# Optimization experiments

Measured on AMD Instinct MI355X. Metric: run time of the kernel, lower is better.

Reference implementation:

```python
import jax, jax.numpy as jnp
import numpy as np

B, S, L, D, H, F, V = 8, 1024, 12, 768, 12, 3072, 21128
TITLE_LEN, CONTENTS_LEN = 64, 960
DH = D // H
NEG_INF = -1e9


def setup_inputs() -> dict:
    key = jax.random.key(0)
    ks = jax.random.split(key, 14)
    p = lambda k, shape: (0.02 * jax.random.normal(k, shape)).astype(jnp.float32)
    return {
        "x": jax.random.randint(ks[0], (B, S), 0, V),
        "y": jax.random.randint(ks[1], (B, CONTENTS_LEN), 0, V),
        "word_emb": p(ks[2], (V, D)),
        "pos_emb": p(ks[3], (S, D)),
        "type_emb": p(ks[4], (2, D)),
        "emb_ln_g": jnp.ones((D,), jnp.float32),
        "emb_ln_b": jnp.zeros((D,), jnp.float32),
        "Wq": p(ks[5], (L, D, D)), "bq": jnp.zeros((L, D), jnp.float32),
        "Wk": p(ks[6], (L, D, D)), "bk": jnp.zeros((L, D), jnp.float32),
        "Wv": p(ks[7], (L, D, D)), "bv": jnp.zeros((L, D), jnp.float32),
        "Wo": p(ks[8], (L, D, D)), "bo": jnp.zeros((L, D), jnp.float32),
        "ln1_g": jnp.ones((L, D), jnp.float32), "ln1_b": jnp.zeros((L, D), jnp.float32),
        "W1": p(ks[9], (L, D, F)), "b1": jnp.zeros((L, F), jnp.float32),
        "W2": p(ks[10], (L, F, D)), "b2": jnp.zeros((L, D), jnp.float32),
        "ln2_g": jnp.ones((L, D), jnp.float32), "ln2_b": jnp.zeros((L, D), jnp.float32),
        "cls_W": p(ks[11], (D, V)), "cls_b": jnp.zeros((V,), jnp.float32),
    }


def _ln(x, g, b):
    m = x.mean(-1, keepdims=True)
    v = jnp.mean((x - m) ** 2, -1, keepdims=True)
    return (x - m) * jax.lax.rsqrt(v + 1e-12) * g + b


def _forward(x, y, word_emb, pos_emb, type_emb, emb_ln_g, emb_ln_b,
             Wq, bq, Wk, bk, Wv, bv, Wo, bo, ln1_g, ln1_b,
             W1, b1, W2, b2, ln2_g, ln2_b, cls_W, cls_b):
    # prefix-LM mask: causal (tril) except fully-visible title block [S,S]
    mask = jnp.tril(jnp.ones((S, S), jnp.float32))
    mask = mask.at[:TITLE_LEN, :TITLE_LEN].set(1.0)
    bias = (1.0 - mask) * NEG_INF  # additive attention bias

    h = word_emb[x] + pos_emb[None, :, :] + type_emb[0]  # [B,S,D]
    h = _ln(h, emb_ln_g, emb_ln_b)

    scale = 1.0 / np.sqrt(DH).astype(np.float32)

    def step(h, p):
        Wq_, bq_, Wk_, bk_, Wv_, bv_, Wo_, bo_, g1, bb1, W1_, bf1, W2_, bf2, g2, bb2 = p
        q = (h @ Wq_ + bq_).reshape(B, S, H, DH)
        k = (h @ Wk_ + bk_).reshape(B, S, H, DH)
        v = (h @ Wv_ + bv_).reshape(B, S, H, DH)
        scores = jnp.einsum('bqhd,bkhd->bhqk', q, k) * scale + bias  # [B,H,S,S]
        a = jax.nn.softmax(scores, axis=-1)
        ctx = jnp.einsum('bhqk,bkhd->bqhd', a, v).reshape(B, S, D)
        h = _ln(h + ctx @ Wo_ + bo_, g1, bb1)
        ffn = jax.nn.gelu(h @ W1_ + bf1, approximate=False) @ W2_ + bf2
        h = _ln(h + ffn, g2, bb2)
        return h, None

    h, _ = jax.lax.scan(step, h, (Wq, bq, Wk, bk, Wv, bv, Wo, bo,
                                  ln1_g, ln1_b, W1, b1, W2, b2, ln2_g, ln2_b))

    logits = h[:, -CONTENTS_LEN:, :] @ cls_W + cls_b  # [B,C,V]
    logp = jax.nn.log_softmax(logits, axis=-1)
    valid = (y != -100)
    yc = jnp.where(valid, y, 0)
    nll = -jnp.take_along_axis(logp, yc[..., None], axis=-1)[..., 0]
    return jnp.sum(nll * valid) / jnp.maximum(jnp.sum(valid), 1)


def reference(x, y, word_emb, pos_emb, type_emb, emb_ln_g, emb_ln_b,
              Wq, bq, Wk, bk, Wv, bv, Wo, bo, ln1_g, ln1_b,
              W1, b1, W2, b2, ln2_g, ln2_b, cls_W, cls_b):
    return _forward(x, y, word_emb, pos_emb, type_emb, emb_ln_g, emb_ln_b,
                    Wq, bq, Wk, bk, Wv, bv, Wo, bo, ln1_g, ln1_b,
                    W1, b1, W2, b2, ln2_g, ln2_b, cls_W, cls_b)
```

## Files before the change

kernel.cpp:

```cpp
#include <hip/hip_runtime.h>

#define BB 8
#define SS 1024
#define LL 12
#define DD 768
#define HH 12
#define FF 3072
#define VV 21128
#define DH 64
#define CLEN 960
#define NROWS (BB * CLEN)
#define TOKS (BB * SS)
#define NQKV 2304
#define QKW 1536

typedef __attribute__((ext_vector_type(8))) short bh8;
typedef __attribute__((ext_vector_type(4))) float f32x4;
typedef __attribute__((ext_vector_type(4))) unsigned short us4;

__device__ __forceinline__ float bf2f(unsigned short u) {
    union { unsigned int i; float f; } c; c.i = ((unsigned int)u) << 16; return c.f;
}
__device__ __forceinline__ unsigned short f2bf(float f) {
    union { float f; unsigned int i; } c; c.f = f;
    unsigned int r = c.i + 0x7fffu + ((c.i >> 16) & 1u);
    return (unsigned short)(r >> 16);
}

#define GLOAD16(gsrc, ldst)                                                              \
    __builtin_amdgcn_global_load_lds((const __attribute__((address_space(1))) unsigned int*)(gsrc), \
                                     (__attribute__((address_space(3))) unsigned int*)(ldst), 16, 0, 0)

__device__ __forceinline__ float bsum256(float v, float* red) {
#pragma unroll
    for (int o = 32; o; o >>= 1) v += __shfl_down(v, o);
    if ((threadIdx.x & 63) == 0) red[threadIdx.x >> 6] = v;
    __syncthreads();
    float r = red[0] + red[1] + red[2] + red[3];
    __syncthreads();
    return r;
}

__global__ void transpose_f32_bf16(const float* __restrict__ in, unsigned short* __restrict__ out,
                                   int R, int C) {
    __shared__ float tile[32][33];
    int c0 = blockIdx.x << 5, r0 = blockIdx.y << 5;
    int tx = threadIdx.x, ty = threadIdx.y;
    for (int i = ty; i < 32; i += 8) {
        int r = r0 + i, c = c0 + tx;
        if (r < R && c < C) tile[i][tx] = in[(size_t)r * C + c];
    }
    __syncthreads();
    for (int i = ty; i < 32; i += 8) {
        int oc = c0 + i, orr = r0 + tx;
        if (oc < C && orr < R) out[(size_t)oc * R + orr] = f2bf(tile[tx][i]);
    }
}

__global__ void transpose_layer(const float* __restrict__ Wq, const float* __restrict__ Wk,
                                const float* __restrict__ Wv, const float* __restrict__ Wo,
                                const float* __restrict__ W1, const float* __restrict__ W2,
                                unsigned short* __restrict__ wqkvT, unsigned short* __restrict__ woT,
                                unsigned short* __restrict__ w1T, unsigned short* __restrict__ w2T) {
    __shared__ float tile[32][33];
    int t = blockIdx.x;
    const float* src;
    unsigned short* dst;
    int R, C, txt, tt;
    if (t < 1728) {
        int which = t / 576; tt = t % 576;
        src = which == 0 ? Wq : (which == 1 ? Wk : Wv);
        dst = wqkvT + (size_t)which * DD * DD; R = DD; C = DD; txt = 24;
    } else if (t < 2304) {
        tt = t - 1728; src = Wo; dst = woT; R = DD; C = DD; txt = 24;
    } else if (t < 4608) {
        tt = t - 2304; src = W1; dst = w1T; R = DD; C = FF; txt = 96;
    } else {
        tt = t - 4608; src = W2; dst = w2T; R = FF; C = DD; txt = 24;
    }
    int c0 = (tt % txt) << 5, r0 = (tt / txt) << 5;
    int tx = threadIdx.x, ty = threadIdx.y;
    for (int i = ty; i < 32; i += 8) tile[i][tx] = src[(size_t)(r0 + i) * C + c0 + tx];
    __syncthreads();
    for (int i = ty; i < 32; i += 8) dst[(size_t)(c0 + i) * R + r0 + tx] = f2bf(tile[tx][i]);
}

__global__ void concat_bias_all(const float* __restrict__ bq, const float* __restrict__ bk,
                                const float* __restrict__ bv, float* __restrict__ out) {
    int i = blockIdx.x * 256 + threadIdx.x;
    if (i >= LL * NQKV) return;
    int l = i / NQKV, c = i % NQKV;
    float v = c < DD ? bq[(size_t)l * DD + c]
                     : (c < 2 * DD ? bk[(size_t)l * DD + c - DD] : bv[(size_t)l * DD + c - 2 * DD]);
    out[i] = v;
}

__global__ __launch_bounds__(256) void embed_ln(const int* __restrict__ x, const float* __restrict__ we,
                                                const float* __restrict__ pe, const float* __restrict__ te,
                                                const float* __restrict__ g, const float* __restrict__ be,
                                                unsigned short* __restrict__ hb) {
    int row = blockIdx.x;
    int s = row & (SS - 1);
    int tok = x[row];
    int tid = threadIdx.x;
    __shared__ float red[4];
    float v[3];
#pragma unroll
    for (int i = 0; i < 3; i++) {
        int c = tid + i * 256;
        v[i] = we[(size_t)tok * DD + c] + pe[(size_t)s * DD + c] + te[c];
    }
    float mean = bsum256(v[0] + v[1] + v[2], red) * (1.f / DD);
    float d0 = v[0] - mean, d1 = v[1] - mean, d2 = v[2] - mean;
    float var = bsum256(d0 * d0 + d1 * d1 + d2 * d2, red) * (1.f / DD);
    float inv = rsqrtf(var + 1e-12f);
    size_t base = (size_t)row * DD;
#pragma unroll
    for (int i = 0; i < 3; i++) {
        int c = tid + i * 256;
        hb[base + c] = f2bf((v[i] - mean) * inv * g[c] + be[c]);
    }
}

__global__ __launch_bounds__(256) void add_ln(const unsigned short* __restrict__ res,
                                              const unsigned short* __restrict__ t,
                                              const float* __restrict__ g, const float* __restrict__ be,
                                              unsigned short* __restrict__ outb) {
    int row = blockIdx.x;
    int tid = threadIdx.x;
    __shared__ float red[4];
    size_t base = (size_t)row * DD;
    float v[3];
#pragma unroll
    for (int i = 0; i < 3; i++) {
        int c = tid + i * 256;
        v[i] = bf2f(res[base + c]) + bf2f(t[base + c]);
    }
    float mean = bsum256(v[0] + v[1] + v[2], red) * (1.f / DD);
    float d0 = v[0] - mean, d1 = v[1] - mean, d2 = v[2] - mean;
    float var = bsum256(d0 * d0 + d1 * d1 + d2 * d2, red) * (1.f / DD);
    float inv = rsqrtf(var + 1e-12f);
#pragma unroll
    for (int i = 0; i < 3; i++) {
        int c = tid + i * 256;
        outb[base + c] = f2bf((v[i] - mean) * inv * g[c] + be[c]);
    }
}

template <int MODE>
__global__ __launch_bounds__(256) void gemm128(const unsigned short* __restrict__ A,
                                               const unsigned short* __restrict__ BT,
                                               const float* __restrict__ bias, void* __restrict__ Cp,
                                               int M, int N, int K, int ldc,
                                               unsigned short* __restrict__ vt_out,
                                               const int* __restrict__ yv,
                                               float* __restrict__ stS, float* __restrict__ stT) {
    __shared__ __align__(16) unsigned short As[2][128 * 32];
    __shared__ __align__(16) unsigned short Bs[2][128 * 32];
    const int tid = threadIdx.x;
    const int lane = tid & 63, w = tid >> 6;
    const int fr = lane & 15, fg = lane >> 4;
    const int wr = w >> 1, wc = w & 1;
    const int m0 = blockIdx.y << 7, n0 = blockIdx.x << 7;
    const int srow = lane >> 2;
    const int skcol = (lane & 3) << 3;

    int arow0 = m0 + (w * 2 + 0) * 16 + srow;
    int arow1 = m0 + (w * 2 + 1) * 16 + srow;
    int brow0 = n0 + (w * 2 + 0) * 16 + srow;
    int brow1 = n0 + (w * 2 + 1) * 16 + srow;
    if (brow0 >= N) brow0 = N - 1;
    if (brow1 >= N) brow1 = N - 1;
    const unsigned short* aptr0 = A + (size_t)arow0 * K + skcol;
    const unsigned short* aptr1 = A + (size_t)arow1 * K + skcol;
    const unsigned short* bptr0 = BT + (size_t)brow0 * K + skcol;
    const unsigned short* bptr1 = BT + (size_t)brow1 * K + skcol;

    auto stage = [&](int bf, int k0) {
        GLOAD16(aptr0 + k0, &As[bf][(w * 2 + 0) * 512]);
        GLOAD16(aptr1 + k0, &As[bf][(w * 2 + 1) * 512]);
        GLOAD16(bptr0 + k0, &Bs[bf][(w * 2 + 0) * 512]);
        GLOAD16(bptr1 + k0, &Bs[bf][(w * 2 + 1) * 512]);
    };

    f32x4 acc[4][4] = {};
    stage(0, 0);
    __syncthreads();
    int cur = 0;
    for (int k0 = 0; k0 < K; k0 += 32) {
        if (k0 + 32 < K) stage(cur ^ 1, k0 + 32);
        bh8 a[4], b[4];
#pragma unroll
        for (int mi = 0; mi < 4; mi++) a[mi] = *(const bh8*)&As[cur][(wr * 64 + mi * 16 + fr) * 32 + fg * 8];
#pragma unroll
        for (int ni = 0; ni < 4; ni++) b[ni] = *(const bh8*)&Bs[cur][(wc * 64 + ni * 16 + fr) * 32 + fg * 8];
        __builtin_amdgcn_s_setprio(1);
#pragma unroll
        for (int mi = 0; mi < 4; mi++)
#pragma unroll
            for (int ni = 0; ni < 4; ni++)
                acc[mi][ni] = __builtin_amdgcn_mfma_f32_16x16x32_bf16(a[mi], b[ni], acc[mi][ni], 0, 0, 0);
        __builtin_amdgcn_s_setprio(0);
        __syncthreads();
        cur ^= 1;
    }

    unsigned short* Cb = (unsigned short*)Cp;
#pragma unroll
    for (int mi = 0; mi < 4; mi++) {
        int rbase = m0 + wr * 64 + mi * 16 + fg * 4;
        if (MODE == 3) {
            float e[4] = {0.f, 0.f, 0.f, 0.f};
            int yr[4];
#pragma unroll
            for (int r = 0; r < 4; r++) yr[r] = yv[rbase + r];
#pragma unroll
            for (int ni = 0; ni < 4; ni++) {
                int col = n0 + wc * 64 + ni * 16 + fr;
                if (col < N) {
                    float bb = bias[col];
#pragma unroll
                    for (int r = 0; r < 4; r++) {
                        float v = acc[mi][ni][r] + bb;
                        e[r] += __expf(v);
                        if (col == yr[r]) stT[rbase + r] = v;
                    }
                }
            }
#pragma unroll
            for (int r = 0; r < 4; r++) {
#pragma unroll
                for (int off = 1; off < 16; off <<= 1) e[r] += __shfl_xor(e[r], off);
                if (fr == 0) atomicAdd(&stS[rbase + r], e[r]);
            }
        } else {
#pragma unroll
            for (int ni = 0; ni < 4; ni++) {
                int col = n0 + wc * 64 + ni * 16 + fr;
                if (MODE == 4) {
                    float bb = bias[col];
                    if (col < 2 * DD) {
#pragma unroll
                        for (int r = 0; r < 4; r++)
                            Cb[(size_t)(rbase + r) * QKW + col] = f2bf(acc[mi][ni][r] + bb);
                    } else {
                        int g = col - 2 * DD, h = g >> 6, d = g & 63;
                        int bi = rbase >> 10, s0 = rbase & 1023;
                        us4 val;
#pragma unroll
                        for (int r = 0; r < 4; r++) val[r] = f2bf(acc[mi][ni][r] + bb);
                        *(us4*)&vt_out[(((size_t)bi * HH + h) * DH + d) * SS + s0] = val;
                    }
                } else if (col < N) {
                    float bb = bias[col];
#pragma unroll
                    for (int r = 0; r < 4; r++) {
                        float v = acc[mi][ni][r] + bb;
                        if (MODE == 2) v = 0.5f * v * (1.0f + erff(v * 0.70710678118f));
                        Cb[(size_t)(rbase + r) * ldc + col] = f2bf(v);
                    }
                }
            }
        }
    }
}

__global__ __launch_bounds__(256) void flash_attn(const unsigned short* __restrict__ qkbuf,
                                                  const unsigned short* __restrict__ VT,
                                                  unsigned short* __restrict__ ctxb) {
    const int qt = (int)gridDim.x - 1 - blockIdx.x;
    const int h = blockIdx.y, b = blockIdx.z;
    const int tid = threadIdx.x;
    const int lane = tid & 63, w = tid >> 6;
    const int fr = lane & 15, fg = lane >> 4;
    __shared__ unsigned short Qs[64][68];
    __shared__ unsigned short Ks[64][68];
    __shared__ unsigned short Vt[64][68];
    __shared__ unsigned short Ps[4][16][68];

    const int srow = tid >> 2, sd0 = (tid & 3) << 4;
    {
        const unsigned short* src = qkbuf + (size_t)(b * SS + qt * 64 + srow) * QKW + h * 64 + sd0;
        *(bh8*)&Qs[srow][sd0] = *(const bh8*)src;
        *(bh8*)&Qs[srow][sd0 + 8] = *(const bh8*)(src + 8);
    }

    const unsigned short* kbase = qkbuf + (size_t)(b * SS + srow) * QKW + DD + h * 64 + sd0;
    const unsigned short* vbase = VT + (((size_t)b * HH + h) * DH + srow) * SS + sd0;

    bh8 kr0, kr1, vr0, vr1;
    auto ld_reg = [&](int kt) {
        const unsigned short* ks = kbase + (size_t)(kt * 64) * QKW;
        kr0 = *(const bh8*)ks;
        kr1 = *(const bh8*)(ks + 8);
        const unsigned short* vs = vbase + kt * 64;
        vr0 = *(const bh8*)vs;
        vr1 = *(const bh8*)(vs + 8);
    };

    f32x4 o[4] = {};
    float m[4], l[4];
#pragma unroll
    for (int r = 0; r < 4; r++) { m[r] = -3e30f; l[r] = 0.f; }

    const int nkt = (qt == 0) ? 1 : qt + 1;
    ld_reg(0);
    for (int kt = 0; kt < nkt; kt++) {
        __syncthreads();
        *(bh8*)&Ks[srow][sd0] = kr0;
        *(bh8*)&Ks[srow][sd0 + 8] = kr1;
        *(bh8*)&Vt[srow][sd0] = vr0;
        *(bh8*)&Vt[srow][sd0 + 8] = vr1;
        if (kt + 1 < nkt) ld_reg(kt + 1);
        __syncthreads();

        f32x4 s[4] = {};
        bh8 a0 = *(const bh8*)&Qs[w * 16 + fr][fg * 8];
        bh8 a1 = *(const bh8*)&Qs[w * 16 + fr][32 + fg * 8];
        __builtin_amdgcn_s_setprio(1);
#pragma unroll
        for (int cf = 0; cf < 4; cf++) {
            bh8 b0 = *(const bh8*)&Ks[cf * 16 + fr][fg * 8];
            bh8 b1 = *(const bh8*)&Ks[cf * 16 + fr][32 + fg * 8];
            s[cf] = __builtin_amdgcn_mfma_f32_16x16x32_bf16(a0, b0, s[cf], 0, 0, 0);
            s[cf] = __builtin_amdgcn_mfma_f32_16x16x32_bf16(a1, b1, s[cf], 0, 0, 0);
        }
        __builtin_amdgcn_s_setprio(0);

        const bool diag = (qt > 0) && (kt == qt);
#pragma unroll
        for (int cf = 0; cf < 4; cf++) {
#pragma unroll
            for (int r = 0; r < 4; r++) {
                float v = s[cf][r] * 0.125f;
                if (diag) {
                    int key = cf * 16 + fr;
                    int qrow = w * 16 + fg * 4 + r;
                    if (key > qrow) v = -1e30f;
                }
                s[cf][r] = v;
            }
        }
        float sc[4], mn[4];
#pragma unroll
        for (int r = 0; r < 4; r++) {
            float v = fmaxf(fmaxf(s[0][r], s[1][r]), fmaxf(s[2][r], s[3][r]));
#pragma unroll
            for (int off = 1; off < 16; off <<= 1) v = fmaxf(v, __shfl_xor(v, off));
            mn[r] = fmaxf(m[r], v);
            sc[r] = __expf(m[r] - mn[r]);
            m[r] = mn[r];
        }
#pragma unroll
        for (int cf = 0; cf < 4; cf++) {
#pragma unroll
            for (int r = 0; r < 4; r++) s[cf][r] = __expf(s[cf][r] - mn[r]);
        }
#pragma unroll
        for (int r = 0; r < 4; r++) {
            float v = s[0][r] + s[1][r] + s[2][r] + s[3][r];
#pragma unroll
            for (int off = 1; off < 16; off <<= 1) v += __shfl_xor(v, off);
            l[r] = l[r] * sc[r] + v;
        }
#pragma unroll
        for (int df = 0; df < 4; df++) {
#pragma unroll
            for (int r = 0; r < 4; r++) o[df][r] *= sc[r];
        }
#pragma unroll
        for (int cf = 0; cf < 4; cf++) {
#pragma unroll
            for (int r = 0; r < 4; r++) Ps[w][fg * 4 + r][cf * 16 + fr] = f2bf(s[cf][r]);
        }
        bh8 pa0 = *(const bh8*)&Ps[w][fr][fg * 8];
        bh8 pa1 = *(const bh8*)&Ps[w][fr][32 + fg * 8];
        __builtin_amdgcn_s_setprio(1);
#pragma unroll
        for (int df = 0; df < 4; df++) {
            bh8 vb0 = *(const bh8*)&Vt[df * 16 + fr][fg * 8];
            bh8 vb1 = *(const bh8*)&Vt[df * 16 + fr][32 + fg * 8];
            o[df] = __builtin_amdgcn_mfma_f32_16x16x32_bf16(pa0, vb0, o[df], 0, 0, 0);
            o[df] = __builtin_amdgcn_mfma_f32_16x16x32_bf16(pa1, vb1, o[df], 0, 0, 0);
        }
        __builtin_amdgcn_s_setprio(0);
    }
#pragma unroll
    for (int df = 0; df < 4; df++) {
#pragma unroll
        for (int r = 0; r < 4; r++) {
            int q = qt * 64 + w * 16 + fg * 4 + r;
            float v = o[df][r] / l[r];
            ctxb[(((size_t)b * SS + q) * HH + h) * DH + df * 16 + fr] = f2bf(v);
        }
    }
}

__global__ void gather_rows(const unsigned short* __restrict__ hb, unsigned short* __restrict__ hc) {
    int idx = blockIdx.x * 256 + threadIdx.x;
    if (idx >= NROWS * (DD / 8)) return;
    int g = idx / (DD / 8), c8 = (idx % (DD / 8)) * 8;
    int b = g / CLEN, cc = g % CLEN;
    *(bh8*)&hc[(size_t)g * DD + c8] = *(const bh8*)&hb[((size_t)(b * SS + 64 + cc)) * DD + c8];
}

__global__ void init_state(float* stS, float* stT) {
    int i = blockIdx.x * 256 + threadIdx.x;
    if (i < NROWS) { stS[i] = 0.f; stT[i] = 0.f; }
}

__global__ __launch_bounds__(256) void final_reduce(const float* __restrict__ stS,
                                                    const float* __restrict__ stT, const int* __restrict__ y,
                                                    float* __restrict__ out) {
    int tid = threadIdx.x;
    float s = 0.f, c = 0.f;
    for (int i = tid; i < NROWS; i += 256) {
        if (y[i] != -100) {
            s += logf(stS[i]) - stT[i];
            c += 1.f;
        }
    }
    __shared__ float red[4];
    float gs = bsum256(s, red);
    float gc = bsum256(c, red);
    if (tid == 0) out[0] = gs / fmaxf(gc, 1.f);
}

extern "C" void kernel_launch(void* const* d_in, const int* in_sizes, int n_in,
                              void* d_out, int out_size, void* d_ws, size_t ws_size,
                              hipStream_t stream) {
    const int* x = (const int*)d_in[0];
    const int* y = (const int*)d_in[1];
    const float* we = (const float*)d_in[2];
    const float* pe = (const float*)d_in[3];
    const float* te = (const float*)d_in[4];
    const float* eg = (const float*)d_in[5];
    const float* eb = (const float*)d_in[6];
    const float* Wq = (const float*)d_in[7];
    const float* bq = (const float*)d_in[8];
    const float* Wk = (const float*)d_in[9];
    const float* bk = (const float*)d_in[10];
    const float* Wv = (const float*)d_in[11];
    const float* bv = (const float*)d_in[12];
    const float* Wo = (const float*)d_in[13];
    const float* bo = (const float*)d_in[14];
    const float* g1 = (const float*)d_in[15];
    const float* b1n = (const float*)d_in[16];
    const float* W1 = (const float*)d_in[17];
    const float* b1 = (const float*)d_in[18];
    const float* W2 = (const float*)d_in[19];
    const float* b2 = (const float*)d_in[20];
    const float* g2 = (const float*)d_in[21];
    const float* b2n = (const float*)d_in[22];
    const float* clsW = (const float*)d_in[23];
    const float* clsb = (const float*)d_in[24];
    float* out = (float*)d_out;

    char* ws = (char*)d_ws;
    size_t off = 0;
    auto alloc = [&](size_t n) {
        void* p = ws + off;
        off += n;
        off = (off + 255) & ~(size_t)255;
        return p;
    };
    unsigned short* hb   = (unsigned short*)alloc((size_t)TOKS * DD * 2);
    unsigned short* h1b  = (unsigned short*)alloc((size_t)TOKS * DD * 2);
    unsigned short* tmpb = (unsigned short*)alloc((size_t)TOKS * DD * 2);
    unsigned short* qkbuf = (unsigned short*)alloc((size_t)TOKS * QKW * 2);
    unsigned short* vtb  = (unsigned short*)alloc((size_t)TOKS * DD * 2);
    unsigned short* ctxb = (unsigned short*)alloc((size_t)TOKS * DD * 2);
    unsigned short* ffnb = (unsigned short*)alloc((size_t)TOKS * FF * 2);
    unsigned short* wqkvT = (unsigned short*)alloc((size_t)NQKV * DD * 2);
    unsigned short* woT = (unsigned short*)alloc((size_t)DD * DD * 2);
    unsigned short* w1T = (unsigned short*)alloc((size_t)DD * FF * 2);
    unsigned short* w2T = (unsigned short*)alloc((size_t)DD * FF * 2);
    unsigned short* clsT = (unsigned short*)alloc((size_t)VV * DD * 2);
    unsigned short* hc = (unsigned short*)alloc((size_t)NROWS * DD * 2);
    float* bqkv = (float*)alloc((size_t)LL * NQKV * 4);
    float* stS = (float*)alloc(NROWS * 4);
    float* stT = (float*)alloc(NROWS * 4);

    dim3 tb(32, 8);
    transpose_f32_bf16<<<dim3((VV + 31) / 32, DD / 32), tb, 0, stream>>>(clsW, clsT, DD, VV);
    concat_bias_all<<<(LL * NQKV + 255) / 256, 256, 0, stream>>>(bq, bk, bv, bqkv);
    embed_ln<<<TOKS, 256, 0, stream>>>(x, we, pe, te, eg, eb, hb);

    for (int l = 0; l < LL; l++) {
        transpose_layer<<<6912, tb, 0, stream>>>(Wq + (size_t)l * DD * DD, Wk + (size_t)l * DD * DD,
                                                 Wv + (size_t)l * DD * DD, Wo + (size_t)l * DD * DD,
                                                 W1 + (size_t)l * DD * FF, W2 + (size_t)l * FF * DD,
                                                 wqkvT, woT, w1T, w2T);

        gemm128<4><<<dim3(NQKV / 128, TOKS / 128), 256, 0, stream>>>(hb, wqkvT, bqkv + (size_t)l * NQKV,
                                                                     qkbuf, TOKS, NQKV, DD, NQKV, vtb,
                                                                     nullptr, nullptr, nullptr);

        flash_attn<<<dim3(SS / 64, HH, BB), 256, 0, stream>>>(qkbuf, vtb, ctxb);

        gemm128<1><<<dim3(DD / 128, TOKS / 128), 256, 0, stream>>>(ctxb, woT, bo + (size_t)l * DD, tmpb,
                                                                   TOKS, DD, DD, DD, nullptr,
                                                                   nullptr, nullptr, nullptr);
        add_ln<<<TOKS, 256, 0, stream>>>(hb, tmpb, g1 + (size_t)l * DD, b1n + (size_t)l * DD, h1b);

        gemm128<2><<<dim3(FF / 128, TOKS / 128), 256, 0, stream>>>(h1b, w1T, b1 + (size_t)l * FF, ffnb,
                                                                   TOKS, FF, DD, FF, nullptr,
                                                                   nullptr, nullptr, nullptr);
        gemm128<1><<<dim3(DD / 128, TOKS / 128), 256, 0, stream>>>(ffnb, w2T, b2 + (size_t)l * DD, tmpb,
                                                                   TOKS, DD, FF, DD, nullptr,
                                                                   nullptr, nullptr, nullptr);
        add_ln<<<TOKS, 256, 0, stream>>>(h1b, tmpb, g2 + (size_t)l * DD, b2n + (size_t)l * DD, hb);
    }

    gather_rows<<<(NROWS * (DD / 8) + 255) / 256, 256, 0, stream>>>(hb, hc);
    init_state<<<(NROWS + 255) / 256, 256, 0, stream>>>(stS, stT);
    gemm128<3><<<dim3((VV + 127) / 128, NROWS / 128), 256, 0, stream>>>(hc, clsT, clsb, nullptr,
                                                                        NROWS, VV, DD, VV, nullptr,
                                                                        y, stS, stT);
    final_reduce<<<1, 256, 0, stream>>>(stS, stT, y, out);
}
```

Baseline: 4.653 ms.

## Swizzle GEMM tile order for XCD/L2 locality and pair causal attention q-tiles

GEMM blocks are remapped so that consecutive blocks on each XCD cover a band of M tiles across N, with the goal of better L2 reuse of A and B tiles. Flash attention now launches half as many blocks, and each processes a short and a long q-tile (15-bx and bx) to balance the causal triangular work across blocks. The trade-offs are extra index arithmetic, and half the attention grid size, which may reduce occupancy and parallelism.

```diff
diff --git a/kernel.cpp b/kernel.cpp
--- a/kernel.cpp
+++ b/kernel.cpp
@@ -151,7 +151,7 @@
 __global__ __launch_bounds__(256) void gemm128(const unsigned short* __restrict__ A,
                                                const unsigned short* __restrict__ BT,
                                                const float* __restrict__ bias, void* __restrict__ Cp,
-                                               int M, int N, int K, int ldc,
+                                               int M, int N, int K, int ldc, int SM,
                                                unsigned short* __restrict__ vt_out,
                                                const int* __restrict__ yv,
                                                float* __restrict__ stS, float* __restrict__ stT) {
@@ -161,7 +161,17 @@
     const int lane = tid & 63, w = tid >> 6;
     const int fr = lane & 15, fg = lane >> 4;
     const int wr = w >> 1, wc = w & 1;
-    const int m0 = blockIdx.y << 7, n0 = blockIdx.x << 7;
+
+    const int Nt = gridDim.x;
+    const int flat = blockIdx.y * Nt + blockIdx.x;
+    const int per8 = (Nt * gridDim.y) >> 3;
+    const int virt = (flat & 7) * per8 + (flat >> 3);
+    const int bandSz = SM * Nt;
+    const int band = virt / bandSz, rem = virt - band * bandSz;
+    const int nt = rem / SM;
+    const int mt = band * SM + (rem - nt * SM);
+    const int m0 = mt << 7, n0 = nt << 7;
+
     const int srow = lane >> 2;
     const int skcol = (lane & 3) << 3;
 
@@ -268,7 +278,7 @@
 __global__ __launch_bounds__(256) void flash_attn(const unsigned short* __restrict__ qkbuf,
                                                   const unsigned short* __restrict__ VT,
                                                   unsigned short* __restrict__ ctxb) {
-    const int qt = (int)gridDim.x - 1 - blockIdx.x;
+    const int bx = blockIdx.x;
     const int h = blockIdx.y, b = blockIdx.z;
     const int tid = threadIdx.x;
     const int lane = tid & 63, w = tid >> 6;
@@ -279,12 +289,6 @@
     __shared__ unsigned short Ps[4][16][68];
 
     const int srow = tid >> 2, sd0 = (tid & 3) << 4;
-    {
-        const unsigned short* src = qkbuf + (size_t)(b * SS + qt * 64 + srow) * QKW + h * 64 + sd0;
-        *(bh8*)&Qs[srow][sd0] = *(const bh8*)src;
-        *(bh8*)&Qs[srow][sd0 + 8] = *(const bh8*)(src + 8);
-    }
-
     const unsigned short* kbase = qkbuf + (size_t)(b * SS + srow) * QKW + DD + h * 64 + sd0;
     const unsigned short* vbase = VT + (((size_t)b * HH + h) * DH + srow) * SS + sd0;
 
@@ -298,100 +302,110 @@
         vr1 = *(const bh8*)(vs + 8);
     };
 
-    f32x4 o[4] = {};
-    float m[4], l[4];
-#pragma unroll
-    for (int r = 0; r < 4; r++) { m[r] = -3e30f; l[r] = 0.f; }
-
-    const int nkt = (qt == 0) ? 1 : qt + 1;
-    ld_reg(0);
-    for (int kt = 0; kt < nkt; kt++) {
+    for (int half = 0; half < 2; half++) {
+        const int qt = (half == 0) ? 15 - bx : bx;
         __syncthreads();
-        *(bh8*)&Ks[srow][sd0] = kr0;
-        *(bh8*)&Ks[srow][sd0 + 8] = kr1;
-        *(bh8*)&Vt[srow][sd0] = vr0;
-        *(bh8*)&Vt[srow][sd0 + 8] = vr1;
-        if (kt + 1 < nkt) ld_reg(kt + 1);
-        __syncthreads();
-
-        f32x4 s[4] = {};
-        bh8 a0 = *(const bh8*)&Qs[w * 16 + fr][fg * 8];
-        bh8 a1 = *(const bh8*)&Qs[w * 16 + fr][32 + fg * 8];
-        __builtin_amdgcn_s_setprio(1);
-#pragma unroll
-        for (int cf = 0; cf < 4; cf++) {
-            bh8 b0 = *(const bh8*)&Ks[cf * 16 + fr][fg * 8];
-            bh8 b1 = *(const bh8*)&Ks[cf * 16 + fr][32 + fg * 8];
-            s[cf] = __builtin_amdgcn_mfma_f32_16x16x32_bf16(a0, b0, s[cf], 0, 0, 0);
-            s[cf] = __builtin_amdgcn_mfma_f32_16x16x32_bf16(a1, b1, s[cf], 0, 0, 0);
+        {
+            const unsigned short* src = qkbuf + (size_t)(b * SS + qt * 64 + srow) * QKW + h * 64 + sd0;
+            *(bh8*)&Qs[srow][sd0] = *(const bh8*)src;
+            *(bh8*)&Qs[srow][sd0 + 8] = *(const bh8*)(src + 8);
         }
-        __builtin_amdgcn_s_setprio(0);
-
-        const bool diag = (qt > 0) && (kt == qt);
-#pragma unroll
-        for (int cf = 0; cf < 4; cf++) {
+
+        f32x4 o[4] = {};
+        float m[4], l[4];
+#pragma unroll
+        for (int r = 0; r < 4; r++) { m[r] = -3e30f; l[r] = 0.f; }
+
+        const int nkt = (qt == 0) ? 1 : qt + 1;
+        ld_reg(0);
+        for (int kt = 0; kt < nkt; kt++) {
+            __syncthreads();
+            *(bh8*)&Ks[srow][sd0] = kr0;
+            *(bh8*)&Ks[srow][sd0 + 8] = kr1;
+            *(bh8*)&Vt[srow][sd0] = vr0;
+            *(bh8*)&Vt[srow][sd0 + 8] = vr1;
+            if (kt + 1 < nkt) ld_reg(kt + 1);
+            __syncthreads();
+
+            f32x4 s[4] = {};
+            bh8 a0 = *(const bh8*)&Qs[w * 16 + fr][fg * 8];
+            bh8 a1 = *(const bh8*)&Qs[w * 16 + fr][32 + fg * 8];
+            __builtin_amdgcn_s_setprio(1);
+#pragma unroll
+            for (int cf = 0; cf < 4; cf++) {
+                bh8 b0 = *(const bh8*)&Ks[cf * 16 + fr][fg * 8];
+                bh8 b1 = *(const bh8*)&Ks[cf * 16 + fr][32 + fg * 8];
+                s[cf] = __builtin_amdgcn_mfma_f32_16x16x32_bf16(a0, b0, s[cf], 0, 0, 0);
+                s[cf] = __builtin_amdgcn_mfma_f32_16x16x32_bf16(a1, b1, s[cf], 0, 0, 0);
+            }
+            __builtin_amdgcn_s_setprio(0);
+
+            const bool diag = (qt > 0) && (kt == qt);
+#pragma unroll
+            for (int cf = 0; cf < 4; cf++) {
+#pragma unroll
+                for (int r = 0; r < 4; r++) {
+                    float v = s[cf][r] * 0.125f;
+                    if (diag) {
+                        int key = cf * 16 + fr;
+                        int qrow = w * 16 + fg * 4 + r;
+                        if (key > qrow) v = -1e30f;
+                    }
+                    s[cf][r] = v;
+                }
+            }
+            float sc[4], mn[4];
 #pragma unroll
             for (int r = 0; r < 4; r++) {
-                float v = s[cf][r] * 0.125f;
-                if (diag) {
-                    int key = cf * 16 + fr;
-                    int qrow = w * 16 + fg * 4 + r;
-                    if (key > qrow) v = -1e30f;
-                }
-                s[cf][r] = v;
-            }
+                float v = fmaxf(fmaxf(s[0][r], s[1][r]), fmaxf(s[2][r], s[3][r]));
+#pragma unroll
+                for (int off = 1; off < 16; off <<= 1) v = fmaxf(v, __shfl_xor(v, off));
+                mn[r] = fmaxf(m[r], v);
+                sc[r] = __expf(m[r] - mn[r]);
+                m[r] = mn[r];
+            }
+#pragma unroll
+            for (int cf = 0; cf < 4; cf++) {
+#pragma unroll
+                for (int r = 0; r < 4; r++) s[cf][r] = __expf(s[cf][r] - mn[r]);
+            }
+#pragma unroll
+            for (int r = 0; r < 4; r++) {
+                float v = s[0][r] + s[1][r] + s[2][r] + s[3][r];
+#pragma unroll
+                for (int off = 1; off < 16; off <<= 1) v += __shfl_xor(v, off);
+                l[r] = l[r] * sc[r] + v;
+            }
+#pragma unroll
+            for (int df = 0; df < 4; df++) {
+#pragma unroll
+                for (int r = 0; r < 4; r++) o[df][r] *= sc[r];
+            }
+#pragma unroll
+            for (int cf = 0; cf < 4; cf++) {
+#pragma unroll
+                for (int r = 0; r < 4; r++) Ps[w][fg * 4 + r][cf * 16 + fr] = f2bf(s[cf][r]);
+            }
+            bh8 pa0 = *(const bh8*)&Ps[w][fr][fg * 8];
+            bh8 pa1 = *(const bh8*)&Ps[w][fr][32 + fg * 8];
+            __builtin_amdgcn_s_setprio(1);
+#pragma unroll
+            for (int df = 0; df < 4; df++) {
+                bh8 vb0 = *(const bh8*)&Vt[df * 16 + fr][fg * 8];
+                bh8 vb1 = *(const bh8*)&Vt[df * 16 + fr][32 + fg * 8];
+                o[df] = __builtin_amdgcn_mfma_f32_16x16x32_bf16(pa0, vb0, o[df], 0, 0, 0);
+                o[df] = __builtin_amdgcn_mfma_f32_16x16x32_bf16(pa1, vb1, o[df], 0, 0, 0);
+            }
+            __builtin_amdgcn_s_setprio(0);
         }
-        float sc[4], mn[4];
-#pragma unroll
-        for (int r = 0; r < 4; r++) {
-            float v = fmaxf(fmaxf(s[0][r], s[1][r]), fmaxf(s[2][r], s[3][r]));
-#pragma unroll
-            for (int off = 1; off < 16; off <<= 1) v = fmaxf(v, __shfl_xor(v, off));
-            mn[r] = fmaxf(m[r], v);
-            sc[r] = __expf(m[r] - mn[r]);
-            m[r] = mn[r];
-        }
-#pragma unroll
-        for (int cf = 0; cf < 4; cf++) {
-#pragma unroll
-            for (int r = 0; r < 4; r++) s[cf][r] = __expf(s[cf][r] - mn[r]);
-        }
-#pragma unroll
-        for (int r = 0; r < 4; r++) {
-            float v = s[0][r] + s[1][r] + s[2][r] + s[3][r];
-#pragma unroll
-            for (int off = 1; off < 16; off <<= 1) v += __shfl_xor(v, off);
-            l[r] = l[r] * sc[r] + v;
-        }
 #pragma unroll
         for (int df = 0; df < 4; df++) {
 #pragma unroll
-            for (int r = 0; r < 4; r++) o[df][r] *= sc[r];
-        }
-#pragma unroll
-        for (int cf = 0; cf < 4; cf++) {
-#pragma unroll
-            for (int r = 0; r < 4; r++) Ps[w][fg * 4 + r][cf * 16 + fr] = f2bf(s[cf][r]);
-        }
-        bh8 pa0 = *(const bh8*)&Ps[w][fr][fg * 8];
-        bh8 pa1 = *(const bh8*)&Ps[w][fr][32 + fg * 8];
-        __builtin_amdgcn_s_setprio(1);
-#pragma unroll
-        for (int df = 0; df < 4; df++) {
-            bh8 vb0 = *(const bh8*)&Vt[df * 16 + fr][fg * 8];
-            bh8 vb1 = *(const bh8*)&Vt[df * 16 + fr][32 + fg * 8];
-            o[df] = __builtin_amdgcn_mfma_f32_16x16x32_bf16(pa0, vb0, o[df], 0, 0, 0);
-            o[df] = __builtin_amdgcn_mfma_f32_16x16x32_bf16(pa1, vb1, o[df], 0, 0, 0);
-        }
-        __builtin_amdgcn_s_setprio(0);
-    }
-#pragma unroll
-    for (int df = 0; df < 4; df++) {
-#pragma unroll
-        for (int r = 0; r < 4; r++) {
-            int q = qt * 64 + w * 16 + fg * 4 + r;
-            float v = o[df][r] / l[r];
-            ctxb[(((size_t)b * SS + q) * HH + h) * DH + df * 16 + fr] = f2bf(v);
+            for (int r = 0; r < 4; r++) {
+                int q = qt * 64 + w * 16 + fg * 4 + r;
+                float v = o[df][r] / l[r];
+                ctxb[(((size_t)b * SS + q) * HH + h) * DH + df * 16 + fr] = f2bf(v);
+            }
         }
     }
 }
@@ -493,21 +507,21 @@
                                                  wqkvT, woT, w1T, w2T);
 
         gemm128<4><<<dim3(NQKV / 128, TOKS / 128), 256, 0, stream>>>(hb, wqkvT, bqkv + (size_t)l * NQKV,
-                                                                     qkbuf, TOKS, NQKV, DD, NQKV, vtb,
+                                                                     qkbuf, TOKS, NQKV, DD, NQKV, 8, vtb,
                                                                      nullptr, nullptr, nullptr);
 
-        flash_attn<<<dim3(SS / 64, HH, BB), 256, 0, stream>>>(qkbuf, vtb, ctxb);
+        flash_attn<<<dim3(8, HH, BB), 256, 0, stream>>>(qkbuf, vtb, ctxb);
 
         gemm128<1><<<dim3(DD / 128, TOKS / 128), 256, 0, stream>>>(ctxb, woT, bo + (size_t)l * DD, tmpb,
-                                                                   TOKS, DD, DD, DD, nullptr,
+                                                                   TOKS, DD, DD, DD, 8, nullptr,
                                                                    nullptr, nullptr, nullptr);
         add_ln<<<TOKS, 256, 0, stream>>>(hb, tmpb, g1 + (size_t)l * DD, b1n + (size_t)l * DD, h1b);
 
         gemm128<2><<<dim3(FF / 128, TOKS / 128), 256, 0, stream>>>(h1b, w1T, b1 + (size_t)l * FF, ffnb,
-                                                                   TOKS, FF, DD, FF, nullptr,
+                                                                   TOKS, FF, DD, FF, 8, nullptr,
                                                                    nullptr, nullptr, nullptr);
         gemm128<1><<<dim3(DD / 128, TOKS / 128), 256, 0, stream>>>(ffnb, w2T, b2 + (size_t)l * DD, tmpb,
-                                                                   TOKS, DD, FF, DD, nullptr,
+                                                                   TOKS, DD, FF, DD, 8, nullptr,
                                                                    nullptr, nullptr, nullptr);
         add_ln<<<TOKS, 256, 0, stream>>>(h1b, tmpb, g2 + (size_t)l * DD, b2n + (size_t)l * DD, hb);
     }
@@ -515,7 +529,7 @@
     gather_rows<<<(NROWS * (DD / 8) + 255) / 256, 256, 0, stream>>>(hb, hc);
     init_state<<<(NROWS + 255) / 256, 256, 0, stream>>>(stS, stT);
     gemm128<3><<<dim3((VV + 127) / 128, NROWS / 128), 256, 0, stream>>>(hc, clsT, clsb, nullptr,
-                                                                        NROWS, VV, DD, VV, nullptr,
+                                                                        NROWS, VV, DD, VV, 6, nullptr,
                                                                         y, stS, stT);
     final_reduce<<<1, 256, 0, stream>>>(stS, stT, y, out);
 }
```

Result: faster. 3.868 ms (-16.9%).
